# Kernel tuning notes

Measured on AMD Instinct MI355X. Metric: run time of the kernel, lower is better.

## Reference

```python
import jax, jax.numpy as jnp
from jax import lax
import numpy as np

B = 32768      # batch
D = 256        # input = hidden = output dim
DEPTH = 9      # universal_depth


def setup_inputs() -> dict:
    key = jax.random.key(0)
    ks = jax.random.split(key, 16)
    s = 1.0 / np.sqrt(D)  # keep pre-activations sane
    r = lambda k, shp, sc=s: (jax.random.normal(k, shp, jnp.float32) * sc)
    return {
        "x": jax.random.normal(ks[0], (B, D), jnp.float32),
        "lin0_w": r(ks[1], (D, D)), "lin0_b": r(ks[2], (D,), 0.1),
        "lin1_w": r(ks[3], (D, D)), "lin1_b": r(ks[4], (D,), 0.1),
        "u1_w": jax.random.normal(ks[5], (DEPTH, D, D), jnp.float32),
        "u1_cw": r(ks[6], (D, D)), "u1_cb": r(ks[7], (D,), 0.1),
        "lin2_w": r(ks[8], (D, D)), "lin2_b": r(ks[9], (D,), 0.1),
        "u2_w": jax.random.normal(ks[10], (DEPTH, D, D), jnp.float32),
        "u2_cw": r(ks[11], (D, D)), "u2_cb": r(ks[12], (D,), 0.1),
        "lino_w": r(ks[13], (D, D)), "lino_b": r(ks[14], (D,), 0.1),
    }


def _universal_layer(x, uw, cw, cb):
    """UniversalNeuralLayer.forward, vectorized.

    The circulant 'gate' matrix implements, for state s of length n:
        s'[i] = cos*s[i] - sin*s[(i+1)%n] + sin*s[(i-1)%n]
    Applied 3 times per depth with angles uw[d, j, 0..2] (j = output unit).
    The result is independent of x and of the batch index.
    """
    n = x.shape[1]
    classical = x @ cw + cb                      # [B, n]
    # angle sequence per output j, in (depth, gate) order -> [3*DEPTH, n]
    angles = jnp.transpose(uw[:, :, :3], (0, 2, 1)).reshape(-1, n)
    init = jnp.full((n, n), 1.0 / np.sqrt(n), dtype=x.dtype)  # [n_j, n_state]

    def step(s, ang):
        c = jnp.cos(ang)[:, None]
        sn = jnp.sin(ang)[:, None]
        return c * s + sn * (jnp.roll(s, 1, axis=1) - jnp.roll(s, -1, axis=1)), None

    s, _ = lax.scan(step, init, angles)
    p = s[:, 0] ** 2                             # |state[0]|^2 per output j
    return jnp.tanh(classical + p[None, :])


def reference(x, lin0_w, lin0_b, lin1_w, lin1_b, u1_w, u1_cw, u1_cb,
              lin2_w, lin2_b, u2_w, u2_cw, u2_cb, lino_w, lino_b):
    h = jax.nn.relu(x @ lin0_w.T + lin0_b)
    h = jax.nn.relu(h @ lin1_w.T + lin1_b)
    h = _universal_layer(h, u1_w, u1_cw, u1_cb)
    h = jax.nn.relu(h @ lin2_w.T + lin2_b)
    h = _universal_layer(h, u2_w, u2_cw, u2_cb)
    return jax.nn.relu(h @ lino_w.T + lino_b)
```

## Files before the change

### kernel.cpp

```cpp
#include <hip/hip_runtime.h>
#include <math.h>

#define DD 256

typedef float  f32x4  __attribute__((ext_vector_type(4)));
typedef short  bf16x8 __attribute__((ext_vector_type(8)));

__device__ __forceinline__ unsigned short f2bf(float f) {
    unsigned int u = __float_as_uint(f);
    u = (u + 0x7fffu + ((u >> 16) & 1u)) >> 16;
    return (unsigned short)u;
}
__device__ __forceinline__ float bf2f(unsigned int h16) {
    return __uint_as_float(h16 << 16);
}

__global__ __launch_bounds__(256)
void universal_p_kernel(const float* __restrict__ u1_w,
                        const float* __restrict__ u2_w,
                        float* __restrict__ p_out ) {
    const int j = threadIdx.x;
    const float* uw = blockIdx.x ? u2_w : u1_w;
    float s = 0.0625f;
#pragma unroll
    for (int d = 0; d < 9; ++d)
#pragma unroll
        for (int g = 0; g < 3; ++g)
            s *= cosf(uw[d * DD * DD + j * DD + g]);
    p_out[blockIdx.x * DD + j] = s * s;
}

__global__ __launch_bounds__(256)
void prep_weights(const float* __restrict__ w0, const float* __restrict__ w1,
                  const float* __restrict__ cw1, const float* __restrict__ w2,
                  const float* __restrict__ cw2, const float* __restrict__ wo,
                  unsigned short* __restrict__ wall) {
    const int gid  = blockIdx.x * 256 + threadIdx.x;
    const int mat  = gid >> 13;
    const int rem  = gid & 8191;
    const int wb   = rem >> 11;
    const int rem2 = rem & 2047;
    const int k0   = rem2 >> 8;
    const int rem3 = rem2 & 255;
    const int nt   = rem3 >> 6;
    const int lane = rem3 & 63;
    const int n  = wb * 64 + nt * 16 + (lane & 15);
    const int kb = k0 * 32 + (lane >> 4) * 8;

    const float* src;
    bool tr = false;
    switch (mat) {
        case 0: src = w0; break;
        case 1: src = w1; break;
        case 2: src = cw1; tr = true; break;
        case 3: src = w2; break;
        case 4: src = cw2; tr = true; break;
        default: src = wo; break;
    }
    unsigned short tmp[8];
#pragma unroll
    for (int j = 0; j < 8; ++j) {
        const float v = tr ? src[(kb + j) * DD + n] : src[n * DD + kb + j];
        tmp[j] = f2bf(v);
    }
    *(uint4*)&wall[mat * 65536 + wb * 16384 + k0 * 2048 + nt * 512 + lane * 8] =
        *(const uint4*)tmp;
}

__device__ __forceinline__ int chunk_idx(int m, int kc) {
    return kc * 32 + (m ^ (kc & 7));
}

__device__ __forceinline__ float fast_tanh(float x) {
    const float e = __expf(2.0f * x);
    return 1.0f - 2.0f * __builtin_amdgcn_rcpf(1.0f + e);
}

template <int MODE>
__device__ __forceinline__ void layer_step(uint4* h, bf16x8 (&wr)[2][4],
                                           const unsigned short* __restrict__ W,
                                           const unsigned short* __restrict__ Wn,
                                           const float* __restrict__ bias,
                                           const float* __restrict__ pv) {
    const int tid  = threadIdx.x;
    const int wave = tid >> 6;
    const int lane = tid & 63;
    const int quad = lane >> 4;
    const int l15  = lane & 15;
    const unsigned short* Wb  = W  + wave * 16384 + lane * 8;
    const unsigned short* Wnb = Wn + wave * 16384 + lane * 8;

    f32x4 acc[4][2];
#pragma unroll
    for (int nt = 0; nt < 4; ++nt)
#pragma unroll
        for (int mt = 0; mt < 2; ++mt) acc[nt][mt] = (f32x4){0.f, 0.f, 0.f, 0.f};

    bf16x8 h_f[2][2];
#pragma unroll
    for (int mt = 0; mt < 2; ++mt)
        h_f[0][mt] = *(const bf16x8*)&h[chunk_idx(mt * 16 + l15, quad)];

#pragma unroll
    for (int k0 = 0; k0 < 8; ++k0) {
        const int cur = k0 & 1, nxt = cur ^ 1;
        {
            const unsigned short* ws = (k0 < 7) ? &Wb[(k0 + 1) * 2048] : Wnb;
#pragma unroll
            for (int nt = 0; nt < 4; ++nt)
                wr[nxt][nt] = *(const bf16x8*)&ws[nt * 512];
        }
        if (k0 < 7) {
            const int kc = (k0 + 1) * 4 + quad;
#pragma unroll
            for (int mt = 0; mt < 2; ++mt)
                h_f[nxt][mt] = *(const bf16x8*)&h[chunk_idx(mt * 16 + l15, kc)];
        }
#pragma unroll
        for (int nt = 0; nt < 4; ++nt)
#pragma unroll
            for (int mt = 0; mt < 2; ++mt)
                acc[nt][mt] = __builtin_amdgcn_mfma_f32_16x16x32_bf16(
                    wr[cur][nt], h_f[cur][mt], acc[nt][mt], 0, 0, 0);
    }

    __syncthreads();

    const int nb = wave * 64;
#pragma unroll
    for (int nt = 0; nt < 4; ++nt) {
        const int n0 = nb + nt * 16 + quad * 4;
        f32x4 add = *(const f32x4*)&bias[n0];
        if (MODE == 1) add += *(const f32x4*)&pv[n0];
        const int kc_o = n0 >> 3;
        const int half = quad & 1;
#pragma unroll
        for (int mt = 0; mt < 2; ++mt) {
            const f32x4 v = acc[nt][mt] + add;
            float t0, t1, t2, t3;
            if (MODE == 1) {
                t0 = fast_tanh(v.x); t1 = fast_tanh(v.y);
                t2 = fast_tanh(v.z); t3 = fast_tanh(v.w);
            } else {
                t0 = fmaxf(v.x, 0.f); t1 = fmaxf(v.y, 0.f);
                t2 = fmaxf(v.z, 0.f); t3 = fmaxf(v.w, 0.f);
            }
            uint2 u;
            u.x = (unsigned int)f2bf(t0) | ((unsigned int)f2bf(t1) << 16);
            u.y = (unsigned int)f2bf(t2) | ((unsigned int)f2bf(t3) << 16);
            *(uint2*)((char*)&h[chunk_idx(mt * 16 + l15, kc_o)] + half * 8) = u;
        }
    }
    __syncthreads();
}

__global__ __launch_bounds__(256, 2)
void unet_fused(const float* __restrict__ x,
                const unsigned short* __restrict__ wall,
                const float* __restrict__ b0, const float* __restrict__ b1,
                const float* __restrict__ cb1, const float* __restrict__ b2,
                const float* __restrict__ cb2, const float* __restrict__ bo,
                const float* __restrict__ pbuf,
                float* __restrict__ out) {
    __shared__ uint4 h[1024];
    const int m0 = blockIdx.x * 32;
    const int tid = threadIdx.x;
    const int wave = tid >> 6;
    const int lane = tid & 63;

    bf16x8 wr[2][4];
    {
        const unsigned short* ws = wall + wave * 16384 + lane * 8;
#pragma unroll
        for (int nt = 0; nt < 4; ++nt)
            wr[0][nt] = *(const bf16x8*)&ws[nt * 512];
    }

    const int c4 = tid & 63;
    const int rbase = (tid >> 6) * 8;
    const int kc_s = c4 >> 1;
    const int half_s = c4 & 1;
#pragma unroll
    for (int i = 0; i < 8; ++i) {
        const int row = rbase + i;
        const float4 v = *(const float4*)&x[(size_t)(m0 + row) * DD + c4 * 4];
        uint2 u;
        u.x = (unsigned int)f2bf(v.x) | ((unsigned int)f2bf(v.y) << 16);
        u.y = (unsigned int)f2bf(v.z) | ((unsigned int)f2bf(v.w) << 16);
        *(uint2*)((char*)&h[chunk_idx(row, kc_s)] + half_s * 8) = u;
    }
    __syncthreads();

    layer_step<0>(h, wr, wall + 0 * 65536, wall + 1 * 65536, b0, nullptr);
    layer_step<0>(h, wr, wall + 1 * 65536, wall + 2 * 65536, b1, nullptr);
    layer_step<1>(h, wr, wall + 2 * 65536, wall + 3 * 65536, cb1, pbuf);
    layer_step<0>(h, wr, wall + 3 * 65536, wall + 4 * 65536, b2, nullptr);
    layer_step<1>(h, wr, wall + 4 * 65536, wall + 5 * 65536, cb2, pbuf + 256);
    layer_step<0>(h, wr, wall + 5 * 65536, wall + 0 * 65536, bo, nullptr);

#pragma unroll
    for (int i = 0; i < 8; ++i) {
        const int row = rbase + i;
        const uint2 u = *(const uint2*)((char*)&h[chunk_idx(row, kc_s)] + half_s * 8);
        float4 v;
        v.x = bf2f(u.x & 0xffffu); v.y = bf2f(u.x >> 16);
        v.z = bf2f(u.y & 0xffffu); v.w = bf2f(u.y >> 16);
        *(float4*)&out[(size_t)(m0 + row) * DD + c4 * 4] = v;
    }
}

extern "C" void kernel_launch(void* const* d_in, const int* in_sizes, int n_in,
                              void* d_out, int out_size, void* d_ws, size_t ws_size,
                              hipStream_t stream) {
    const float* x      = (const float*)d_in[0];
    const float* lin0_w = (const float*)d_in[1];
    const float* lin0_b = (const float*)d_in[2];
    const float* lin1_w = (const float*)d_in[3];
    const float* lin1_b = (const float*)d_in[4];
    const float* u1_w   = (const float*)d_in[5];
    const float* u1_cw  = (const float*)d_in[6];
    const float* u1_cb  = (const float*)d_in[7];
    const float* lin2_w = (const float*)d_in[8];
    const float* lin2_b = (const float*)d_in[9];
    const float* u2_w   = (const float*)d_in[10];
    const float* u2_cw  = (const float*)d_in[11];
    const float* u2_cb  = (const float*)d_in[12];
    const float* lino_w = (const float*)d_in[13];
    const float* lino_b = (const float*)d_in[14];

    float* out = (float*)d_out;
    unsigned short* wall = (unsigned short*)d_ws;
    float* pbuf = (float*)((char*)d_ws + 6 * 65536 * 2);

    universal_p_kernel<<<dim3(2), dim3(256), 0, stream>>>(u1_w, u2_w, pbuf);
    prep_weights<<<dim3(192), dim3(256), 0, stream>>>(
        lin0_w, lin1_w, u1_cw, lin2_w, u2_cw, lino_w, wall);
    unet_fused<<<dim3(1024), dim3(256), 0, stream>>>(
        x, wall, lin0_b, lin1_b, u1_cb, lin2_b, u2_cb, lino_b, pbuf, out);
}
```

Measured before the change: 154.8 us.

## Use 64-row tiles with 8 waves, deeper weight prefetch, merged prep kernels

The fused MLP kernel now processes 64 rows per block with 512 threads (8 waves). Each wave computes 32 output columns by 64 rows, so every weight fragment loaded from global memory feeds four MFMAs instead of two, which halves weight traffic per row. Weight register prefetch is deepened to three k-steps ahead. __syncthreads is replaced by an LDS-only waitcnt plus s_barrier, and the two small prep kernels are merged into one launch. Costs: more LDS per block, more accumulator and fragment registers under a 4-blocks launch bound, and possible occupancy or spill pressure.

```diff
diff --git a/kernel.cpp b/kernel.cpp
--- a/kernel.cpp
+++ b/kernel.cpp
@@ -16,25 +16,24 @@
 }
 
 __global__ __launch_bounds__(256)
-void universal_p_kernel(const float* __restrict__ u1_w,
-                        const float* __restrict__ u2_w,
-                        float* __restrict__ p_out ) {
-    const int j = threadIdx.x;
-    const float* uw = blockIdx.x ? u2_w : u1_w;
-    float s = 0.0625f;
-#pragma unroll
-    for (int d = 0; d < 9; ++d)
-#pragma unroll
-        for (int g = 0; g < 3; ++g)
-            s *= cosf(uw[d * DD * DD + j * DD + g]);
-    p_out[blockIdx.x * DD + j] = s * s;
-}
-
-__global__ __launch_bounds__(256)
-void prep_weights(const float* __restrict__ w0, const float* __restrict__ w1,
-                  const float* __restrict__ cw1, const float* __restrict__ w2,
-                  const float* __restrict__ cw2, const float* __restrict__ wo,
-                  unsigned short* __restrict__ wall) {
+void prep_all(const float* __restrict__ w0, const float* __restrict__ w1,
+              const float* __restrict__ cw1, const float* __restrict__ w2,
+              const float* __restrict__ cw2, const float* __restrict__ wo,
+              const float* __restrict__ u1_w, const float* __restrict__ u2_w,
+              unsigned short* __restrict__ wall, float* __restrict__ p_out) {
+    if (blockIdx.x >= 192) {
+        const int j = threadIdx.x;
+        const int which = blockIdx.x - 192;
+        const float* uw = which ? u2_w : u1_w;
+        float s = 0.0625f;
+#pragma unroll
+        for (int d = 0; d < 9; ++d)
+#pragma unroll
+            for (int g = 0; g < 3; ++g)
+                s *= cosf(uw[d * DD * DD + j * DD + g]);
+        p_out[which * DD + j] = s * s;
+        return;
+    }
     const int gid  = blockIdx.x * 256 + threadIdx.x;
     const int mat  = gid >> 13;
     const int rem  = gid & 8191;
@@ -68,7 +67,7 @@
 }
 
 __device__ __forceinline__ int chunk_idx(int m, int kc) {
-    return kc * 32 + (m ^ (kc & 7));
+    return kc * 64 + (m ^ (kc & 7));
 }
 
 __device__ __forceinline__ float fast_tanh(float x) {
@@ -76,67 +75,76 @@
     return 1.0f - 2.0f * __builtin_amdgcn_rcpf(1.0f + e);
 }
 
+__device__ __forceinline__ void lds_barrier() {
+    asm volatile("s_waitcnt lgkmcnt(0)" ::: "memory");
+    __builtin_amdgcn_s_barrier();
+}
+
 template <int MODE>
-__device__ __forceinline__ void layer_step(uint4* h, bf16x8 (&wr)[2][4],
+__device__ __forceinline__ void layer_step(uint4* h, bf16x8 (&wr)[4][2],
                                            const unsigned short* __restrict__ W,
                                            const unsigned short* __restrict__ Wn,
                                            const float* __restrict__ bias,
                                            const float* __restrict__ pv) {
     const int tid  = threadIdx.x;
-    const int wave = tid >> 6;
+    const int wv   = tid >> 6;
     const int lane = tid & 63;
     const int quad = lane >> 4;
     const int l15  = lane & 15;
-    const unsigned short* Wb  = W  + wave * 16384 + lane * 8;
-    const unsigned short* Wnb = Wn + wave * 16384 + lane * 8;
-
-    f32x4 acc[4][2];
-#pragma unroll
-    for (int nt = 0; nt < 4; ++nt)
-#pragma unroll
-        for (int mt = 0; mt < 2; ++mt) acc[nt][mt] = (f32x4){0.f, 0.f, 0.f, 0.f};
-
-    bf16x8 h_f[2][2];
-#pragma unroll
-    for (int mt = 0; mt < 2; ++mt)
+
+    f32x4 acc[2][4];
+#pragma unroll
+    for (int nt = 0; nt < 2; ++nt)
+#pragma unroll
+        for (int mt = 0; mt < 4; ++mt) acc[nt][mt] = (f32x4){0.f, 0.f, 0.f, 0.f};
+
+    bf16x8 h_f[2][4];
+#pragma unroll
+    for (int mt = 0; mt < 4; ++mt)
         h_f[0][mt] = *(const bf16x8*)&h[chunk_idx(mt * 16 + l15, quad)];
 
 #pragma unroll
     for (int k0 = 0; k0 < 8; ++k0) {
-        const int cur = k0 & 1, nxt = cur ^ 1;
         {
-            const unsigned short* ws = (k0 < 7) ? &Wb[(k0 + 1) * 2048] : Wnb;
-#pragma unroll
-            for (int nt = 0; nt < 4; ++nt)
-                wr[nxt][nt] = *(const bf16x8*)&ws[nt * 512];
+            const int t = k0 + 3;
+            const unsigned short* ws = (t < 8) ? &W[t * 2048] : &Wn[(t - 8) * 2048];
+#pragma unroll
+            for (int nt = 0; nt < 2; ++nt)
+                wr[t & 3][nt] = *(const bf16x8*)&ws[nt * 512];
         }
         if (k0 < 7) {
             const int kc = (k0 + 1) * 4 + quad;
 #pragma unroll
-            for (int mt = 0; mt < 2; ++mt)
-                h_f[nxt][mt] = *(const bf16x8*)&h[chunk_idx(mt * 16 + l15, kc)];
+            for (int mt = 0; mt < 4; ++mt)
+                h_f[(k0 + 1) & 1][mt] = *(const bf16x8*)&h[chunk_idx(mt * 16 + l15, kc)];
         }
 #pragma unroll
-        for (int nt = 0; nt < 4; ++nt)
-#pragma unroll
-            for (int mt = 0; mt < 2; ++mt)
+        for (int nt = 0; nt < 2; ++nt)
+#pragma unroll
+            for (int mt = 0; mt < 4; ++mt)
                 acc[nt][mt] = __builtin_amdgcn_mfma_f32_16x16x32_bf16(
-                    wr[cur][nt], h_f[cur][mt], acc[nt][mt], 0, 0, 0);
-    }
-
-    __syncthreads();
-
-    const int nb = wave * 64;
-#pragma unroll
-    for (int nt = 0; nt < 4; ++nt) {
+                    wr[k0 & 3][nt], h_f[k0 & 1][mt], acc[nt][mt], 0, 0, 0);
+    }
+
+    const int nb = wv * 32;
+    f32x4 addv[2];
+#pragma unroll
+    for (int nt = 0; nt < 2; ++nt) {
         const int n0 = nb + nt * 16 + quad * 4;
-        f32x4 add = *(const f32x4*)&bias[n0];
-        if (MODE == 1) add += *(const f32x4*)&pv[n0];
+        addv[nt] = *(const f32x4*)&bias[n0];
+        if (MODE == 1) addv[nt] += *(const f32x4*)&pv[n0];
+    }
+
+    lds_barrier();
+
+#pragma unroll
+    for (int nt = 0; nt < 2; ++nt) {
+        const int n0   = nb + nt * 16 + quad * 4;
         const int kc_o = n0 >> 3;
         const int half = quad & 1;
 #pragma unroll
-        for (int mt = 0; mt < 2; ++mt) {
-            const f32x4 v = acc[nt][mt] + add;
+        for (int mt = 0; mt < 4; ++mt) {
+            const f32x4 v = acc[nt][mt] + addv[nt];
             float t0, t1, t2, t3;
             if (MODE == 1) {
                 t0 = fast_tanh(v.x); t1 = fast_tanh(v.y);
@@ -151,10 +159,11 @@
             *(uint2*)((char*)&h[chunk_idx(mt * 16 + l15, kc_o)] + half * 8) = u;
         }
     }
-    __syncthreads();
-}
-
-__global__ __launch_bounds__(256, 2)
+
+    lds_barrier();
+}
+
+__global__ __launch_bounds__(512, 4)
 void unet_fused(const float* __restrict__ x,
                 const unsigned short* __restrict__ wall,
                 const float* __restrict__ b0, const float* __restrict__ b1,
@@ -162,23 +171,25 @@
                 const float* __restrict__ cb2, const float* __restrict__ bo,
                 const float* __restrict__ pbuf,
                 float* __restrict__ out) {
-    __shared__ uint4 h[1024];
-    const int m0 = blockIdx.x * 32;
-    const int tid = threadIdx.x;
-    const int wave = tid >> 6;
+    __shared__ uint4 h[2048];
+    const int m0   = blockIdx.x * 64;
+    const int tid  = threadIdx.x;
+    const int wv   = tid >> 6;
     const int lane = tid & 63;
 
-    bf16x8 wr[2][4];
-    {
-        const unsigned short* ws = wall + wave * 16384 + lane * 8;
-#pragma unroll
-        for (int nt = 0; nt < 4; ++nt)
-            wr[0][nt] = *(const bf16x8*)&ws[nt * 512];
-    }
-
-    const int c4 = tid & 63;
-    const int rbase = (tid >> 6) * 8;
-    const int kc_s = c4 >> 1;
+    const unsigned short* WB =
+        wall + (wv >> 1) * 16384 + (wv & 1) * 1024 + lane * 8;
+
+    bf16x8 wr[4][2];
+#pragma unroll
+    for (int t = 0; t < 3; ++t)
+#pragma unroll
+        for (int nt = 0; nt < 2; ++nt)
+            wr[t][nt] = *(const bf16x8*)&WB[t * 2048 + nt * 512];
+
+    const int c4     = tid & 63;
+    const int rbase  = wv * 8;
+    const int kc_s   = c4 >> 1;
     const int half_s = c4 & 1;
 #pragma unroll
     for (int i = 0; i < 8; ++i) {
@@ -189,19 +200,20 @@
         u.y = (unsigned int)f2bf(v.z) | ((unsigned int)f2bf(v.w) << 16);
         *(uint2*)((char*)&h[chunk_idx(row, kc_s)] + half_s * 8) = u;
     }
-    __syncthreads();
-
-    layer_step<0>(h, wr, wall + 0 * 65536, wall + 1 * 65536, b0, nullptr);
-    layer_step<0>(h, wr, wall + 1 * 65536, wall + 2 * 65536, b1, nullptr);
-    layer_step<1>(h, wr, wall + 2 * 65536, wall + 3 * 65536, cb1, pbuf);
-    layer_step<0>(h, wr, wall + 3 * 65536, wall + 4 * 65536, b2, nullptr);
-    layer_step<1>(h, wr, wall + 4 * 65536, wall + 5 * 65536, cb2, pbuf + 256);
-    layer_step<0>(h, wr, wall + 5 * 65536, wall + 0 * 65536, bo, nullptr);
+    lds_barrier();
+
+    layer_step<0>(h, wr, WB + 0 * 65536, WB + 1 * 65536, b0, nullptr);
+    layer_step<0>(h, wr, WB + 1 * 65536, WB + 2 * 65536, b1, nullptr);
+    layer_step<1>(h, wr, WB + 2 * 65536, WB + 3 * 65536, cb1, pbuf);
+    layer_step<0>(h, wr, WB + 3 * 65536, WB + 4 * 65536, b2, nullptr);
+    layer_step<1>(h, wr, WB + 4 * 65536, WB + 5 * 65536, cb2, pbuf + 256);
+    layer_step<0>(h, wr, WB + 5 * 65536, WB + 0 * 65536, bo, nullptr);
 
 #pragma unroll
     for (int i = 0; i < 8; ++i) {
         const int row = rbase + i;
-        const uint2 u = *(const uint2*)((char*)&h[chunk_idx(row, kc_s)] + half_s * 8);
+        const uint2 u =
+            *(const uint2*)((char*)&h[chunk_idx(row, kc_s)] + half_s * 8);
         float4 v;
         v.x = bf2f(u.x & 0xffffu); v.y = bf2f(u.x >> 16);
         v.z = bf2f(u.y & 0xffffu); v.w = bf2f(u.y >> 16);
@@ -232,9 +244,8 @@
     unsigned short* wall = (unsigned short*)d_ws;
     float* pbuf = (float*)((char*)d_ws + 6 * 65536 * 2);
 
-    universal_p_kernel<<<dim3(2), dim3(256), 0, stream>>>(u1_w, u2_w, pbuf);
-    prep_weights<<<dim3(192), dim3(256), 0, stream>>>(
-        lin0_w, lin1_w, u1_cw, lin2_w, u2_cw, lino_w, wall);
-    unet_fused<<<dim3(1024), dim3(256), 0, stream>>>(
+    prep_all<<<dim3(194), dim3(256), 0, stream>>>(
+        lin0_w, lin1_w, u1_cw, lin2_w, u2_cw, lino_w, u1_w, u2_w, wall, pbuf);
+    unet_fused<<<dim3(512), dim3(512), 0, stream>>>(
         x, wall, lin0_b, lin1_b, u1_cb, lin2_b, u2_cb, lino_b, pbuf, out);
 }
```

Result: faster. 144.9 us (-6.4%).
